# Kernel tuning notes

Measured on AMD Instinct MI355X. Metric: run time of the kernel, lower is better.

Reference implementation:

```python
import jax, jax.numpy as jnp
import numpy as np

HIDDEN = 768
HEADS = 12
HEAD_DIM = HIDDEN // HEADS
GRID_SIZE = 5
SPLINE_ORDER = 3
COEFF = GRID_SIZE + SPLINE_ORDER  # 8
ROPE_THETA = 10000.0


def _make_grid():
    # uniform grid over [-1, 1] extended by spline_order knots on each side
    h = 2.0 / GRID_SIZE
    return jnp.arange(-SPLINE_ORDER, GRID_SIZE + SPLINE_ORDER + 1, dtype=jnp.float32) * h - 1.0


def _b_splines(x2d, grid):
    # x2d: (N, in) -> bases: (N, in, COEFF) via Cox-de Boor recursion
    xg = x2d[..., None]  # (N, in, 1)
    bases = ((xg >= grid[:-1]) & (xg < grid[1:])).astype(x2d.dtype)
    for k in range(1, SPLINE_ORDER + 1):
        left = (xg - grid[: -(k + 1)]) / (grid[k:-1] - grid[: -(k + 1)]) * bases[..., :-1]
        right = (grid[k + 1:] - xg) / (grid[k + 1:] - grid[1:-k]) * bases[..., 1:]
        bases = left + right
    return bases


def _kan_linear(x, base_w, spline_w, scaler, grid):
    # x: (..., in); base_w: (out, in); spline_w: (out, in, COEFF); scaler: (out, in)
    orig = x.shape
    x2d = x.reshape(-1, orig[-1])
    base = jax.nn.silu(x2d) @ base_w.T
    bases = _b_splines(x2d, grid)                       # (N, in, COEFF)
    scaled_w = spline_w * scaler[..., None]             # (out, in, COEFF)
    spline = jnp.einsum('nic,oic->no', bases, scaled_w)
    return (base + spline).reshape(*orig[:-1], -1)


def _rope(q, k):
    # q, k: (B, H, S, D); GPT-NeoX style rotate_half RoPE
    S, D = q.shape[-2], q.shape[-1]
    inv_freq = 1.0 / (ROPE_THETA ** (jnp.arange(0, D, 2, dtype=jnp.float32) / D))
    t = jnp.arange(S, dtype=jnp.float32)
    freqs = jnp.outer(t, inv_freq)                      # (S, D/2)
    emb = jnp.concatenate([freqs, freqs], axis=-1)      # (S, D)
    cos, sin = jnp.cos(emb), jnp.sin(emb)

    def rot_half(u):
        u1, u2 = u[..., : D // 2], u[..., D // 2:]
        return jnp.concatenate([-u2, u1], axis=-1)

    q = q * cos + rot_half(q) * sin
    k = k * cos + rot_half(k) * sin
    return q, k


def setup_inputs() -> dict:
    key = jax.random.key(0)
    ks = jax.random.split(key, 12)
    s_base = 1.0 / np.sqrt(HIDDEN)
    s_spline = 0.1 / np.sqrt(HIDDEN)
    d = {
        'x': jax.random.normal(ks[0], (4, 1024, HIDDEN), jnp.float32) * 0.5,
        'q_base_w': jax.random.normal(ks[1], (HIDDEN, HIDDEN), jnp.float32) * s_base,
        'q_spline_w': jax.random.normal(ks[2], (HIDDEN, HIDDEN, COEFF), jnp.float32) * s_spline,
        'q_scaler': 1.0 + 0.1 * jax.random.normal(ks[3], (HIDDEN, HIDDEN), jnp.float32),
        'k_base_w': jax.random.normal(ks[4], (HIDDEN, HIDDEN), jnp.float32) * s_base,
        'k_spline_w': jax.random.normal(ks[5], (HIDDEN, HIDDEN, COEFF), jnp.float32) * s_spline,
        'k_scaler': 1.0 + 0.1 * jax.random.normal(ks[6], (HIDDEN, HIDDEN), jnp.float32),
        'v_base_w': jax.random.normal(ks[7], (HIDDEN, HIDDEN), jnp.float32) * s_base,
        'v_spline_w': jax.random.normal(ks[8], (HIDDEN, HIDDEN, COEFF), jnp.float32) * s_spline,
        'v_scaler': 1.0 + 0.1 * jax.random.normal(ks[9], (HIDDEN, HIDDEN), jnp.float32),
        'out_w': jax.random.normal(ks[10], (HIDDEN, HIDDEN), jnp.float32) * s_base,
        'out_b': jnp.zeros((HIDDEN,), jnp.float32),
    }
    return d


def reference(x, q_base_w, q_spline_w, q_scaler, k_base_w, k_spline_w, k_scaler,
              v_base_w, v_spline_w, v_scaler, out_w, out_b):
    B, S, _ = x.shape
    grid = _make_grid()
    q = _kan_linear(x, q_base_w, q_spline_w, q_scaler, grid)
    k = _kan_linear(x, k_base_w, k_spline_w, k_scaler, grid)
    v = _kan_linear(x, v_base_w, v_spline_w, v_scaler, grid)
    # (B, S, H, D) -> (B, H, S, D)
    q = q.reshape(B, S, HEADS, HEAD_DIM).transpose(0, 2, 1, 3)
    k = k.reshape(B, S, HEADS, HEAD_DIM).transpose(0, 2, 1, 3)
    v = v.reshape(B, S, HEADS, HEAD_DIM).transpose(0, 2, 1, 3)
    q, k = _rope(q, k)
    scores = jnp.einsum('bhqd,bhkd->bhqk', q, k) / jnp.sqrt(jnp.float32(HEAD_DIM))
    alphas = jax.nn.softmax(scores, axis=-1)
    attn = jnp.einsum('bhqk,bhkd->bhqd', alphas, v)
    attn = attn.transpose(0, 2, 1, 3).reshape(B, S, HIDDEN)
    return attn @ out_w.T + out_b
```

## Files before the change

### kernel.cpp

```cpp
#include <hip/hip_runtime.h>
#include <hip/hip_bf16.h>
#include <hip/hip_fp16.h>

#define HIDDEN 768
#define NTOK   4096
#define SEQ    1024
#define NBATCH 4
#define NHEADS 12
#define KAUG   (HIDDEN * 9)
#define NQKV   (3 * HIDDEN)

using bf16 = __hip_bfloat16;
using fp16 = __half;
typedef __attribute__((ext_vector_type(4))) float f32x4;
typedef __attribute__((ext_vector_type(8))) short bf16x8;
typedef __attribute__((ext_vector_type(8))) _Float16 h16x8;

__device__ inline void gload_lds16(const void* g, void* l) {
    __builtin_amdgcn_global_load_lds((const __attribute__((address_space(1))) void*)g,
                                     (__attribute__((address_space(3))) void*)l, 16, 0, 0);
}

__global__ __launch_bounds__(256) void prep(const float* __restrict__ x,
        const float* __restrict__ qbw, const float* __restrict__ qsw, const float* __restrict__ qsc,
        const float* __restrict__ kbw, const float* __restrict__ ksw, const float* __restrict__ ksc,
        const float* __restrict__ vbw, const float* __restrict__ vsw, const float* __restrict__ vsc,
        bf16* __restrict__ xa, bf16* __restrict__ wa) {
    int blk = blockIdx.x;
    const int tid = threadIdx.x;
    if (blk < 12288) {
        int gid = blk * 256 + tid;
        float xv = x[gid];
        int n = gid / HIDDEN;
        int i = gid - n * HIDDEN;
        float sil = xv / (1.0f + __expf(-xv));
        float g[12];
#pragma unroll
        for (int k = 0; k < 12; ++k) g[k] = (float)(k - 3) * 0.4f - 1.0f;
        float b[11];
#pragma unroll
        for (int c = 0; c < 11; ++c) b[c] = (xv >= g[c] && xv < g[c + 1]) ? 1.0f : 0.0f;
#pragma unroll
        for (int k = 1; k <= 3; ++k) {
#pragma unroll
            for (int c = 0; c < 11; ++c) {
                if (c < 11 - k) {
                    float left  = (xv - g[c]) / (g[c + k] - g[c]) * b[c];
                    float right = (g[c + k + 1] - xv) / (g[c + k + 1] - g[c + 1]) * b[c + 1];
                    b[c] = left + right;
                }
            }
        }
        bf16* dst = xa + (size_t)n * KAUG + (size_t)i * 9;
        dst[0] = __float2bfloat16(sil);
#pragma unroll
        for (int c = 0; c < 8; ++c) dst[1 + c] = __float2bfloat16(b[c]);
        return;
    }
    blk -= 12288;
    int job = blk / 2304;
    int gid = (blk - job * 2304) * 256 + tid;
    const float* bw = job == 0 ? qbw : (job == 1 ? kbw : vbw);
    const float* sw = job == 0 ? qsw : (job == 1 ? ksw : vsw);
    const float* sc = job == 0 ? qsc : (job == 1 ? ksc : vsc);
    float bwv = bw[gid];
    float scv = sc[gid];
    bf16* dst = wa + (size_t)job * HIDDEN * KAUG + (size_t)gid * 9;
    dst[0] = __float2bfloat16(bwv);
#pragma unroll
    for (int c = 0; c < 8; ++c)
        dst[1 + c] = __float2bfloat16(sw[(size_t)gid * 8 + c] * scv);
}

template <int KSPLIT>
__global__ __launch_bounds__(512, 2) void gemm256_8ph(const bf16* __restrict__ A,
                                                      const bf16* __restrict__ B,
                                                      fp16* __restrict__ C,
                                                      int M, int N, int K) {
    extern __shared__ char smem[];
    const int tid  = threadIdx.x;
    const int lane = tid & 63;
    const int wave = tid >> 6;
    const int wm = wave >> 2;
    const int wn = wave & 3;

    const int nwg = gridDim.x * gridDim.y;
    const int per = nwg >> 3;
    int lin = blockIdx.y * gridDim.x + blockIdx.x;
    int swz = (lin & 7) * per + (lin >> 3);
    const int row0 = (swz % gridDim.x) * 256;
    const int col0 = (swz / gridDim.x) * 256;

    const int kslice = K / KSPLIT;
    const int koff = blockIdx.z * kslice;
    const int ntiles = kslice >> 6;
    fp16* Cs = C + (size_t)blockIdx.z * M * N;

    const int lr = lane & 15;
    const int lk = (lane >> 4) * 8;
    const int xorv = (lr & 7) << 4;

    f32x4 acc[8][4];
#pragma unroll
    for (int m = 0; m < 8; ++m)
#pragma unroll
        for (int n = 0; n < 4; ++n) acc[m][n] = f32x4{0.f, 0.f, 0.f, 0.f};

    auto stage_half = [&](int buf, int half, int t) {
#pragma unroll
        for (int j = 0; j < 2; ++j) {
            int idx = tid + j * 512;
            int r = idx >> 3;
            int swzc = ((((idx & 7) * 16) ^ ((r & 7) << 4)) >> 1);
            const bf16* src = (half < 2)
                ? A + (size_t)(row0 + half * 128 + r) * K + koff + t * 64 + swzc
                : B + (size_t)(col0 + (half - 2) * 128 + r) * K + koff + t * 64 + swzc;
            gload_lds16(src, smem + ((size_t)(buf * 4 + half) << 14) + idx * 16);
        }
    };
    auto rdA = [&](int buf, int mh, bf16x8 (&af)[4][2]) {
        const char* Ab = smem + ((size_t)(buf * 4 + wm) << 14);
#pragma unroll
        for (int m = 0; m < 4; ++m)
#pragma unroll
            for (int kk = 0; kk < 2; ++kk)
                af[m][kk] = *(const bf16x8*)(Ab + (mh * 64 + m * 16 + lr) * 128 +
                                             (((kk * 32 + lk) * 2) ^ xorv));
    };
    auto rdB = [&](int buf, int nh, bf16x8 (&bf)[2][2]) {
        const char* Bb = smem + ((size_t)(buf * 4 + 2 + (wn >> 1)) << 14);
#pragma unroll
        for (int n = 0; n < 2; ++n)
#pragma unroll
            for (int kk = 0; kk < 2; ++kk)
                bf[n][kk] = *(const bf16x8*)(Bb + ((wn & 1) * 64 + nh * 32 + n * 16 + lr) * 128 +
                                             (((kk * 32 + lk) * 2) ^ xorv));
    };

    stage_half(0, 0, 0); stage_half(0, 1, 0); stage_half(0, 2, 0); stage_half(0, 3, 0);
    stage_half(1, 2, 1); stage_half(1, 3, 1);
    asm volatile("s_waitcnt vmcnt(0)" ::: "memory");
    __builtin_amdgcn_s_barrier();

    bf16x8 af[4][2], bf0[2][2], bf1[2][2];

#define QUAD(MH, NH, BF)                                                         \
    __builtin_amdgcn_s_setprio(1);                                               \
    _Pragma("unroll") for (int m = 0; m < 4; ++m)                                \
        _Pragma("unroll") for (int n = 0; n < 2; ++n)                            \
            _Pragma("unroll") for (int kk = 0; kk < 2; ++kk)                     \
                acc[(MH)*4 + m][(NH)*2 + n] = __builtin_amdgcn_mfma_f32_16x16x32_bf16( \
                    af[m][kk], BF[n][kk], acc[(MH)*4 + m][(NH)*2 + n], 0, 0, 0); \
    __builtin_amdgcn_s_setprio(0);

    for (int u = 0; u < ntiles; ++u) {
        const int buf = u & 1, nbuf = buf ^ 1;
        rdA(buf, 0, af);
        rdB(buf, 0, bf0);
        if (u + 1 < ntiles) stage_half(nbuf, 0, u + 1);
        __builtin_amdgcn_s_barrier();
        asm volatile("s_waitcnt lgkmcnt(0)" ::: "memory");
        __builtin_amdgcn_sched_barrier(0);
        QUAD(0, 0, bf0)
        __builtin_amdgcn_sched_barrier(0);
        __builtin_amdgcn_s_barrier();
        rdB(buf, 1, bf1);
        if (u + 1 < ntiles) stage_half(nbuf, 1, u + 1);
        __builtin_amdgcn_s_barrier();
        asm volatile("s_waitcnt lgkmcnt(0)" ::: "memory");
        __builtin_amdgcn_sched_barrier(0);
        QUAD(0, 1, bf1)
        __builtin_amdgcn_sched_barrier(0);
        __builtin_amdgcn_s_barrier();
        rdA(buf, 1, af);
        if (u + 2 < ntiles) stage_half(buf, 2, u + 2);
        __builtin_amdgcn_s_barrier();
        asm volatile("s_waitcnt lgkmcnt(0)" ::: "memory");
        __builtin_amdgcn_sched_barrier(0);
        QUAD(1, 1, bf1)
        __builtin_amdgcn_sched_barrier(0);
        __builtin_amdgcn_s_barrier();
        if (u + 2 < ntiles) {
            stage_half(buf, 3, u + 2);
            asm volatile("s_waitcnt vmcnt(4)" ::: "memory");
        } else {
            asm volatile("s_waitcnt vmcnt(0)" ::: "memory");
        }
        __builtin_amdgcn_s_barrier();
        __builtin_amdgcn_sched_barrier(0);
        QUAD(1, 0, bf0)
        __builtin_amdgcn_sched_barrier(0);
        __builtin_amdgcn_s_barrier();
    }
#undef QUAD

    const int cr = (lane >> 4) * 4;
    const int cc = lane & 15;
#pragma unroll
    for (int am = 0; am < 8; ++am) {
#pragma unroll
        for (int an = 0; an < 4; ++an) {
            int c = col0 + wn * 64 + an * 16 + cc;
#pragma unroll
            for (int j = 0; j < 4; ++j) {
                int r = row0 + wm * 128 + am * 16 + cr + j;
                Cs[(size_t)r * N + c] = __float2half(acc[am][an][j]);
            }
        }
    }
}

__global__ __launch_bounds__(256) void gemm_bt(const bf16* __restrict__ A,
                                               const bf16* __restrict__ B,
                                               float* __restrict__ C,
                                               const float* __restrict__ bias,
                                               int M, int N, int K) {
    __shared__ __align__(16) bf16 As[2][128][64];
    __shared__ __align__(16) bf16 Bs[2][128][64];
    const int tid  = threadIdx.x;
    const int lane = tid & 63;
    const int wave = tid >> 6;
    const int wr = wave >> 1, wc = wave & 1;

    const int gx = gridDim.x;
    const int per = (gx * gridDim.y) >> 3;
    int lin = blockIdx.y * gx + blockIdx.x;
    int swz = (lin & 7) * per + (lin >> 3);
    const int row0 = (swz % gx) * 128;
    const int col0 = (swz / gx) * 128;

    f32x4 acc[4][4];
#pragma unroll
    for (int m = 0; m < 4; ++m)
#pragma unroll
        for (int n = 0; n < 4; ++n) acc[m][n] = f32x4{0.f, 0.f, 0.f, 0.f};

    const int srow = tid >> 3;
    const int scol = ((((tid & 7) * 16) ^ ((srow & 7) << 4)) >> 1);
    const bf16* aptr = A + (size_t)(row0 + srow) * K + scol;
    const bf16* bptr = B + (size_t)(col0 + srow) * K + scol;

    const int lr = lane & 15;
    const int lk = (lane >> 4) * 8;
    const int xorv = (lr & 7) << 4;
    const int nt = K >> 6;

    auto stage = [&](int buf, int k0) {
        char* adst = (char*)&As[buf][0][0] + tid * 16;
        char* bdst = (char*)&Bs[buf][0][0] + tid * 16;
#pragma unroll
        for (int j = 0; j < 4; ++j)
            gload_lds16(aptr + (size_t)j * 32 * K + k0, adst + j * 4096);
#pragma unroll
        for (int j = 0; j < 4; ++j)
            gload_lds16(bptr + (size_t)j * 32 * K + k0, bdst + j * 4096);
    };

    stage(0, 0);
    asm volatile("s_waitcnt vmcnt(0)" ::: "memory");
    __syncthreads();

    int cur = 0;
    for (int t = 0; t < nt; ++t) {
        if (t + 1 < nt) stage(cur ^ 1, (t + 1) << 6);
        __builtin_amdgcn_s_setprio(1);
#pragma unroll
        for (int kk = 0; kk < 64; kk += 32) {
            const int cb = ((kk + lk) * 2) ^ xorv;
            bf16x8 af[4], bfv[4];
#pragma unroll
            for (int m = 0; m < 4; ++m)
                af[m] = *(const bf16x8*)((char*)&As[cur][0][0] + (wr * 64 + m * 16 + lr) * 128 + cb);
#pragma unroll
            for (int n = 0; n < 4; ++n)
                bfv[n] = *(const bf16x8*)((char*)&Bs[cur][0][0] + (wc * 64 + n * 16 + lr) * 128 + cb);
#pragma unroll
            for (int m = 0; m < 4; ++m)
#pragma unroll
                for (int n = 0; n < 4; ++n)
                    acc[m][n] = __builtin_amdgcn_mfma_f32_16x16x32_bf16(af[m], bfv[n], acc[m][n], 0, 0, 0);
        }
        __builtin_amdgcn_s_setprio(0);
        __builtin_amdgcn_sched_barrier(0);
        if (t + 1 < nt)
            asm volatile("s_waitcnt vmcnt(0)" ::: "memory");
        __builtin_amdgcn_s_barrier();
        __builtin_amdgcn_sched_barrier(0);
        cur ^= 1;
    }

    const int cr = (lane >> 4) * 4;
    const int cc = lane & 15;
#pragma unroll
    for (int m = 0; m < 4; ++m) {
#pragma unroll
        for (int n = 0; n < 4; ++n) {
            int c = col0 + wc * 64 + n * 16 + cc;
            float bv = bias ? bias[c] : 0.0f;
#pragma unroll
            for (int j = 0; j < 4; ++j) {
                int r = row0 + wr * 64 + m * 16 + cr + j;
                C[(size_t)r * N + c] = acc[m][n][j] + bv;
            }
        }
    }
}

__global__ __launch_bounds__(256) void rope_vt(const fp16* __restrict__ qkv0,
                                               bf16* __restrict__ qb,
                                               bf16* __restrict__ kb,
                                               bf16* __restrict__ vbT,
                                               const float* __restrict__ ow,
                                               bf16* __restrict__ owb) {
    __shared__ bf16 tile[64][65];
    const fp16* qkv1 = qkv0 + (size_t)NTOK * NQKV;
    const fp16* qkv2 = qkv1 + (size_t)NTOK * NQKV;
    int blk = blockIdx.x;
    const int tid = threadIdx.x;
    if (blk < 6144) {
        int gid = blk * 256 + tid;
        int d = gid & 31;
        int h = (gid >> 5) % NHEADS;
        int n = gid / (32 * NHEADS);
        int s = n & (SEQ - 1);
        int b = n >> 10;
        float inv = __expf(-(float)d * 0.28782313662425574f);
        float th = (float)s * inv;
        float sn, cs;
        sincosf(th, &sn, &cs);
        size_t src = (size_t)n * NQKV + h * 64 + d;
        auto rd = [&](size_t idx) {
            return __half2float(qkv0[idx]) + __half2float(qkv1[idx]) + __half2float(qkv2[idx]);
        };
        float q0 = rd(src),       q1 = rd(src + 32);
        float k0 = rd(src + 768), k1 = rd(src + 800);
        int bh = b * NHEADS + h;
        size_t dst = ((size_t)bh * SEQ + s) * 64 + d;
        const float QS = 0.18033688011f;
        qb[dst]      = __float2bfloat16((q0 * cs - q1 * sn) * QS);
        qb[dst + 32] = __float2bfloat16((q1 * cs + q0 * sn) * QS);
        kb[dst]      = __float2bfloat16(k0 * cs - k1 * sn);
        kb[dst + 32] = __float2bfloat16(k1 * cs + k0 * sn);
        return;
    }
    blk -= 6144;
    if (blk < 768) {
        int bh = blk >> 4, st = blk & 15;
        int b = bh / NHEADS, h = bh - b * NHEADS;
        {
            int s = tid >> 2, d0 = (tid & 3) * 16;
            size_t src = (size_t)(b * SEQ + st * 64 + s) * NQKV + 1536 + h * 64 + d0;
#pragma unroll
            for (int c = 0; c < 2; ++c) {
                h16x8 a0 = *(const h16x8*)(qkv0 + src + c * 8);
                h16x8 a1 = *(const h16x8*)(qkv1 + src + c * 8);
                h16x8 a2 = *(const h16x8*)(qkv2 + src + c * 8);
#pragma unroll
                for (int j = 0; j < 8; ++j)
                    tile[s][d0 + c * 8 + j] =
                        __float2bfloat16((float)a0[j] + (float)a1[j] + (float)a2[j]);
            }
        }
        __syncthreads();
        {
            int d = tid >> 2, s0 = (tid & 3) * 16;
            bf16 out[16];
#pragma unroll
            for (int i = 0; i < 16; ++i) out[i] = tile[s0 + i][d];
            bf16* dst = vbT + ((size_t)bh * 64 + d) * SEQ + st * 64 + s0;
            *(bf16x8*)(dst)     = *(bf16x8*)&out[0];
            *(bf16x8*)(dst + 8) = *(bf16x8*)&out[8];
        }
        return;
    }
    blk -= 768;
    int gid = blk * 256 + tid;
    owb[gid] = __float2bfloat16(ow[gid]);
}

__global__ __launch_bounds__(256) void attn_mfma(const bf16* __restrict__ qb,
                                                 const bf16* __restrict__ kb,
                                                 const bf16* __restrict__ vbT,
                                                 bf16* __restrict__ attnb) {
    __shared__ __align__(16) bf16 Kls[2][64][64];
    __shared__ __align__(16) bf16 Vt[2][64][64];
    __shared__ __align__(16) bf16 Pls[4][16][72];

    const int tid  = threadIdx.x;
    const int lane = tid & 63;
    const int w    = tid >> 6;
    const int bh   = blockIdx.x;
    const int b    = bh / NHEADS, h = bh - b * NHEADS;
    const int qt   = blockIdx.y;

    const bf16* qhead  = qb  + (size_t)bh * SEQ * 64;
    const char* khead  = (const char*)(kb  + (size_t)bh * SEQ * 64);
    const char* vheadT = (const char*)(vbT + (size_t)bh * 64 * SEQ);

    const int lr = lane & 15;
    const int lg = lane >> 4;
    const int xorv = (lr & 7) << 4;

    bf16x8 qf[2];
    {
        const bf16* qrow = qhead + (size_t)(qt * 64 + w * 16 + lr) * 64 + lg * 8;
        qf[0] = *(const bf16x8*)qrow;
        qf[1] = *(const bf16x8*)(qrow + 32);
    }

    f32x4 oacc[4];
#pragma unroll
    for (int n = 0; n < 4; ++n) oacc[n] = f32x4{0.f, 0.f, 0.f, 0.f};
    float mrun[4], lsum[4];
#pragma unroll
    for (int j = 0; j < 4; ++j) { mrun[j] = -3.0e38f; lsum[j] = 0.0f; }

    auto stage = [&](int bufi, int t) {
#pragma unroll
        for (int j = 0; j < 2; ++j) {
            int idx = tid + j * 256;
            int r = idx >> 3;
            int swz = ((idx & 7) * 16) ^ ((r & 7) << 4);
            gload_lds16(khead + (size_t)(t * 64 + r) * 128 + swz,
                        (char*)&Kls[bufi][0][0] + idx * 16);
            gload_lds16(vheadT + (size_t)r * (SEQ * 2) + t * 128 + swz,
                        (char*)&Vt[bufi][0][0] + idx * 16);
        }
    };

    stage(0, 0);
    asm volatile("s_waitcnt vmcnt(0)" ::: "memory");
    __builtin_amdgcn_s_barrier();

    for (int t = 0; t < SEQ / 64; ++t) {
        const int bufi = t & 1;
        if (t + 1 < SEQ / 64) stage(bufi ^ 1, t + 1);

        f32x4 sacc[4];
#pragma unroll
        for (int n = 0; n < 4; ++n) sacc[n] = f32x4{0.f, 0.f, 0.f, 0.f};
        __builtin_amdgcn_s_setprio(1);
#pragma unroll
        for (int c = 0; c < 2; ++c)
#pragma unroll
            for (int n = 0; n < 4; ++n) {
                bf16x8 kf = *(const bf16x8*)((char*)&Kls[bufi][0][0] +
                                             (n * 16 + lr) * 128 + (((c * 32 + lg * 8) * 2) ^ xorv));
                sacc[n] = __builtin_amdgcn_mfma_f32_16x16x32_bf16(qf[c], kf, sacc[n], 0, 0, 0);
            }
        __builtin_amdgcn_s_setprio(0);

        float rowmax[4];
        bool viol = false;
#pragma unroll
        for (int j = 0; j < 4; ++j) {
            rowmax[j] = fmaxf(fmaxf(sacc[0][j], sacc[1][j]), fmaxf(sacc[2][j], sacc[3][j]));
            viol |= rowmax[j] > mrun[j] + 11.5f;
        }
        if (__ballot(viol) != 0ull) {
#pragma unroll
            for (int j = 0; j < 4; ++j) {
                float mx = rowmax[j];
                mx = fmaxf(mx, __shfl_xor(mx, 1));
                mx = fmaxf(mx, __shfl_xor(mx, 2));
                mx = fmaxf(mx, __shfl_xor(mx, 4));
                mx = fmaxf(mx, __shfl_xor(mx, 8));
                float mnew = fmaxf(mrun[j], mx);
                float csc = exp2f(mrun[j] - mnew);
                mrun[j] = mnew;
                lsum[j] *= csc;
#pragma unroll
                for (int n = 0; n < 4; ++n) oacc[n][j] *= csc;
            }
        }

        float pj[4][4];
#pragma unroll
        for (int j = 0; j < 4; ++j) {
            float p0 = exp2f(sacc[0][j] - mrun[j]);
            float p1 = exp2f(sacc[1][j] - mrun[j]);
            float p2 = exp2f(sacc[2][j] - mrun[j]);
            float p3 = exp2f(sacc[3][j] - mrun[j]);
            pj[0][j] = p0; pj[1][j] = p1; pj[2][j] = p2; pj[3][j] = p3;
            lsum[j] += (p0 + p1) + (p2 + p3);
        }

#pragma unroll
        for (int n = 0; n < 4; ++n)
#pragma unroll
            for (int j = 0; j < 4; ++j)
                Pls[w][lg * 4 + j][n * 16 + lr] = __float2bfloat16(pj[n][j]);

        __builtin_amdgcn_s_setprio(1);
#pragma unroll
        for (int c = 0; c < 2; ++c) {
            bf16x8 pf = *(const bf16x8*)&Pls[w][lr][c * 32 + lg * 8];
#pragma unroll
            for (int n = 0; n < 4; ++n) {
                bf16x8 vf = *(const bf16x8*)((char*)&Vt[bufi][0][0] +
                                             (n * 16 + lr) * 128 + (((c * 32 + lg * 8) * 2) ^ xorv));
                oacc[n] = __builtin_amdgcn_mfma_f32_16x16x32_bf16(pf, vf, oacc[n], 0, 0, 0);
            }
        }
        __builtin_amdgcn_s_setprio(0);

        if (t + 1 < SEQ / 64)
            asm volatile("s_waitcnt vmcnt(0)" ::: "memory");
        __builtin_amdgcn_s_barrier();
    }

#pragma unroll
    for (int j = 0; j < 4; ++j) {
        float l = lsum[j];
        l += __shfl_xor(l, 1);
        l += __shfl_xor(l, 2);
        l += __shfl_xor(l, 4);
        l += __shfl_xor(l, 8);
        float invl = 1.0f / l;
        int tok = b * SEQ + qt * 64 + w * 16 + lg * 4 + j;
        bf16* dst = attnb + (size_t)tok * HIDDEN + h * 64;
#pragma unroll
        for (int n = 0; n < 4; ++n)
            dst[n * 16 + lr] = __float2bfloat16(oacc[n][j] * invl);
    }
}

extern "C" void kernel_launch(void* const* d_in, const int* in_sizes, int n_in,
                              void* d_out, int out_size, void* d_ws, size_t ws_size,
                              hipStream_t stream) {
    const float* x   = (const float*)d_in[0];
    const float* qbw = (const float*)d_in[1];
    const float* qsw = (const float*)d_in[2];
    const float* qsc = (const float*)d_in[3];
    const float* kbw = (const float*)d_in[4];
    const float* ksw = (const float*)d_in[5];
    const float* ksc = (const float*)d_in[6];
    const float* vbw = (const float*)d_in[7];
    const float* vsw = (const float*)d_in[8];
    const float* vsc = (const float*)d_in[9];
    const float* ow  = (const float*)d_in[10];
    const float* ob  = (const float*)d_in[11];

    char* ws = (char*)d_ws;
    size_t off = 0;
    bf16*  xaug = (bf16*)(ws + off); off += (size_t)NTOK * KAUG * 2;
    bf16*  waug = (bf16*)(ws + off); off += (size_t)NQKV * KAUG * 2;
    fp16*  qkvp = (fp16*)(ws + off); off += (size_t)3 * NTOK * NQKV * 2;
    if (off > ws_size) return;

    bf16* attnb = xaug;
    bf16* owb   = (bf16*)((char*)xaug + (8u << 20));
    const size_t headsz = (size_t)NTOK * 64 * NHEADS;
    bf16* qb  = waug;
    bf16* kb  = waug + headsz;
    bf16* vbT = waug + 2 * headsz;

    hipFuncSetAttribute(reinterpret_cast<const void*>(gemm256_8ph<3>),
                        hipFuncAttributeMaxDynamicSharedMemorySize, 131072);

    prep<<<12288 + 3 * 2304, 256, 0, stream>>>(
        x, qbw, qsw, qsc, kbw, ksw, ksc, vbw, vsw, vsc, xaug, waug);

    gemm256_8ph<3><<<dim3(NTOK / 256, NQKV / 256, 3), 512, 131072, stream>>>(
        xaug, waug, qkvp, NTOK, NQKV, KAUG);

    rope_vt<<<6144 + 768 + 2304, 256, 0, stream>>>(qkvp, qb, kb, vbT, ow, owb);
    attn_mfma<<<dim3(NBATCH * NHEADS, SEQ / 64), 256, 0, stream>>>(qb, kb, vbT, attnb);
    gemm_bt<<<dim3(NTOK / 128, HIDDEN / 128), 256, 0, stream>>>(attnb, owb, (float*)d_out, ob, NTOK, HIDDEN, HIDDEN);
}
```

Measured before the change: 275.7 us.

## Stage K/V tiles through registers into single LDS buffer in attention

Replaces the double-buffered direct global-to-LDS loads of K and V tiles with register prefetch of the next tile followed by an explicit LDS write after a barrier, so only one LDS buffer is needed. It also adds a launch-bounds occupancy hint of 4 blocks per SM. The goal is lower LDS use and higher occupancy, at the cost of an extra barrier per iteration, more registers per thread, and serialisation between compute and the LDS write.

Measured after the change: 271.3 us. No clear change (-1.6%).

```diff
diff --git a/kernel.cpp b/kernel.cpp
--- a/kernel.cpp
+++ b/kernel.cpp
@@ -378,12 +378,12 @@
     owb[gid] = __float2bfloat16(ow[gid]);
 }
 
-__global__ __launch_bounds__(256) void attn_mfma(const bf16* __restrict__ qb,
-                                                 const bf16* __restrict__ kb,
-                                                 const bf16* __restrict__ vbT,
-                                                 bf16* __restrict__ attnb) {
-    __shared__ __align__(16) bf16 Kls[2][64][64];
-    __shared__ __align__(16) bf16 Vt[2][64][64];
+__global__ __launch_bounds__(256, 4) void attn_mfma(const bf16* __restrict__ qb,
+                                                    const bf16* __restrict__ kb,
+                                                    const bf16* __restrict__ vbT,
+                                                    bf16* __restrict__ attnb) {
+    __shared__ __align__(16) bf16 Kls[64][64];
+    __shared__ __align__(16) bf16 Vt[64][64];
     __shared__ __align__(16) bf16 Pls[4][16][72];
 
     const int tid  = threadIdx.x;
@@ -401,6 +401,11 @@
     const int lg = lane >> 4;
     const int xorv = (lr & 7) << 4;
 
+    const int r0 = tid >> 3;
+    const int r1 = (tid + 256) >> 3;
+    const int sw0 = ((tid & 7) * 16) ^ ((r0 & 7) << 4);
+    const int sw1 = ((tid & 7) * 16) ^ ((r1 & 7) << 4);
+
     bf16x8 qf[2];
     {
         const bf16* qrow = qhead + (size_t)(qt * 64 + w * 16 + lr) * 64 + lg * 8;
@@ -415,26 +420,28 @@
 #pragma unroll
     for (int j = 0; j < 4; ++j) { mrun[j] = -3.0e38f; lsum[j] = 0.0f; }
 
-    auto stage = [&](int bufi, int t) {
-#pragma unroll
-        for (int j = 0; j < 2; ++j) {
-            int idx = tid + j * 256;
-            int r = idx >> 3;
-            int swz = ((idx & 7) * 16) ^ ((r & 7) << 4);
-            gload_lds16(khead + (size_t)(t * 64 + r) * 128 + swz,
-                        (char*)&Kls[bufi][0][0] + idx * 16);
-            gload_lds16(vheadT + (size_t)r * (SEQ * 2) + t * 128 + swz,
-                        (char*)&Vt[bufi][0][0] + idx * 16);
-        }
+    bf16x8 kst0, kst1, vst0, vst1;
+    auto load_regs = [&](int t) {
+        kst0 = *(const bf16x8*)(khead + (size_t)(t * 64 + r0) * 128 + sw0);
+        kst1 = *(const bf16x8*)(khead + (size_t)(t * 64 + r1) * 128 + sw1);
+        vst0 = *(const bf16x8*)(vheadT + (size_t)r0 * (SEQ * 2) + t * 128 + sw0);
+        vst1 = *(const bf16x8*)(vheadT + (size_t)r1 * (SEQ * 2) + t * 128 + sw1);
     };
-
-    stage(0, 0);
+    auto write_lds = [&]() {
+        *(bf16x8*)((char*)&Kls[0][0] + tid * 16)       = kst0;
+        *(bf16x8*)((char*)&Kls[0][0] + (tid + 256) * 16) = kst1;
+        *(bf16x8*)((char*)&Vt[0][0] + tid * 16)        = vst0;
+        *(bf16x8*)((char*)&Vt[0][0] + (tid + 256) * 16) = vst1;
+    };
+
+    load_regs(0);
     asm volatile("s_waitcnt vmcnt(0)" ::: "memory");
+    write_lds();
+    asm volatile("s_waitcnt lgkmcnt(0)" ::: "memory");
     __builtin_amdgcn_s_barrier();
 
     for (int t = 0; t < SEQ / 64; ++t) {
-        const int bufi = t & 1;
-        if (t + 1 < SEQ / 64) stage(bufi ^ 1, t + 1);
+        if (t + 1 < SEQ / 64) load_regs(t + 1);
 
         f32x4 sacc[4];
 #pragma unroll
@@ -444,7 +451,7 @@
         for (int c = 0; c < 2; ++c)
 #pragma unroll
             for (int n = 0; n < 4; ++n) {
-                bf16x8 kf = *(const bf16x8*)((char*)&Kls[bufi][0][0] +
+                bf16x8 kf = *(const bf16x8*)((char*)&Kls[0][0] +
                                              (n * 16 + lr) * 128 + (((c * 32 + lg * 8) * 2) ^ xorv));
                 sacc[n] = __builtin_amdgcn_mfma_f32_16x16x32_bf16(qf[c], kf, sacc[n], 0, 0, 0);
             }
@@ -497,16 +504,20 @@
             bf16x8 pf = *(const bf16x8*)&Pls[w][lr][c * 32 + lg * 8];
 #pragma unroll
             for (int n = 0; n < 4; ++n) {
-                bf16x8 vf = *(const bf16x8*)((char*)&Vt[bufi][0][0] +
+                bf16x8 vf = *(const bf16x8*)((char*)&Vt[0][0] +
                                              (n * 16 + lr) * 128 + (((c * 32 + lg * 8) * 2) ^ xorv));
                 oacc[n] = __builtin_amdgcn_mfma_f32_16x16x32_bf16(pf, vf, oacc[n], 0, 0, 0);
             }
         }
         __builtin_amdgcn_s_setprio(0);
 
-        if (t + 1 < SEQ / 64)
+        if (t + 1 < SEQ / 64) {
+            __builtin_amdgcn_s_barrier();
             asm volatile("s_waitcnt vmcnt(0)" ::: "memory");
-        __builtin_amdgcn_s_barrier();
+            write_lds();
+            asm volatile("s_waitcnt lgkmcnt(0)" ::: "memory");
+            __builtin_amdgcn_s_barrier();
+        }
     }
 
 #pragma unroll
```
